# Kernel tuning notes

Measured on AMD Instinct MI355X. Metric: run time of the kernel, lower is better.

## Reference

```python
import jax, jax.numpy as jnp
import numpy as np

K = 7
PAD = (K - 1) // 2  # padding=None branch in __init__
STRIDE = 1
N, C, P, H, W = 32, 256, 256, 7, 7


def setup_inputs() -> dict:
    key = jax.random.key(0)
    k1, k2, k3, k4 = jax.random.split(key, 4)
    x = jax.random.normal(k1, (N, C, H, W), dtype=jnp.float32)
    # conv_k = Conv2d(1, planes, 1): weight (P,1,1,1) -> vector Wk, bias bk
    Wk = jax.random.normal(k2, (P,), dtype=jnp.float32) * 0.1
    bk = jax.random.normal(k3, (P,), dtype=jnp.float32) * 0.1
    # conv_adap_kernel bias (its weight is overwritten every forward)
    b_adap = jax.random.normal(k4, (P,), dtype=jnp.float32) * 0.1
    return {"x": x, "Wk": Wk, "bk": bk, "b_adap": b_adap}


def reference(x, Wk, bk, b_adap):
    # Per-sample generated filter: g_k = conv_k(x[i].view(C,1,H,W)) then permute(1,0,2,3)
    # => w[n, p, c, h, w] = x[n, c, h, w] * Wk[p] + bk[p], shape (N, P, C, H, W)
    w = x[:, None, :, :, :] * Wk[None, :, None, None, None] + bk[None, :, None, None, None]

    def conv_one(xi, wi):
        # xi: (C, H, W); wi: (P, C, H, W) -- kernel spatial size == feature map size
        return jax.lax.conv_general_dilated(
            xi[None], wi,
            window_strides=(STRIDE, STRIDE),
            padding=[(PAD, PAD), (PAD, PAD)],
            dimension_numbers=("NCHW", "OIHW", "NCHW"),
        )[0]

    y = jax.vmap(conv_one)(x, w)  # (N, P, Hout, Wout)
    return y + b_adap[None, :, None, None]
```

## Files before the change

### kernel.cpp

```cpp
#include <hip/hip_runtime.h>


#define HW 49

__global__ __launch_bounds__(1024, 4) void adap_fc_kernel(
    const float* __restrict__ x,
    const float* __restrict__ Wk,
    const float* __restrict__ bk,
    const float* __restrict__ ba,
    float* __restrict__ y)
{
    const int bid  = blockIdx.x;
    const int n    = bid & 31;
    const int pg   = bid >> 5;
    const int t    = threadIdx.x;
    const int lane = t & 63;
    const int wg   = (t >> 6) & 3;
    const int q    = t >> 8;

    __shared__ float lx[256 * HW];
    __shared__ float p1[4][25];
    __shared__ float pz[16][HW];
    __shared__ float zz[HW], s1f[HW], s2[HW];
    __shared__ float lwk[32], lbk[32], lba[32];

    const float4* xn4 = (const float4*)(x + (size_t)n * (256 * HW));
    float4* lx4 = (float4*)lx;
    #pragma unroll
    for (int i = 0; i < 3; ++i) lx4[t + i * 1024] = xn4[t + i * 1024];
    if (t < 64) lx4[t + 3072] = xn4[t + 3072];
    if (t < 32) { const int p = pg * 32 + t; lwk[t] = Wk[p]; lbk[t] = bk[p]; lba[t] = ba[p]; }
    __syncthreads();

    const int c = t & 255;
    float v[HW];
    #pragma unroll
    for (int k = 0; k < HW; ++k) v[k] = lx[c * HW + k];

    #pragma unroll
    for (int l = 0; l < 25; ++l) {
        const int lq = (l < 7) ? 0 : (l < 13) ? 1 : (l < 19) ? 2 : 3;
        if (q == lq) {
            const int dh = (l < 4) ? 0 : (l - 4) / 7 + 1;
            const int dw = (l < 4) ? l : (l - 4) % 7 - 3;
            float a = 0.f;
            #pragma unroll
            for (int i = 0; i < 7; ++i) {
                if (i + dh < 0 || i + dh > 6) continue;
                #pragma unroll
                for (int j = 0; j < 7; ++j) {
                    if (j + dw < 0 || j + dw > 6) continue;
                    a += v[(i + dh) * 7 + (j + dw)] * v[i * 7 + j];
                }
            }
            #pragma unroll
            for (int off = 32; off; off >>= 1) a += __shfl_xor(a, off);
            if (lane == 0) p1[wg][l] = a;
        }
    }

    if (t < 784) {
        const int grp = t / 49, pos = t % 49;
        const float* base = lx + (grp * 16) * HW + pos;
        float a0 = 0.f, a1 = 0.f;
        #pragma unroll
        for (int i = 0; i < 16; i += 2) { a0 += base[i * HW]; a1 += base[(i + 1) * HW]; }
        pz[grp][pos] = a0 + a1;
    }
    __syncthreads();

    if (t < HW) {
        float az = 0.f;
        #pragma unroll
        for (int g = 0; g < 16; ++g) az += pz[g][t];
        zz[t] = az;
        int dh = t / 7 - 3, dw = t % 7 - 3;
        if (dh < 0 || (dh == 0 && dw < 0)) { dh = -dh; dw = -dw; }
        const int l = (dh == 0) ? dw : 4 + (dh - 1) * 7 + (dw + 3);
        s1f[t] = p1[0][l] + p1[1][l] + p1[2][l] + p1[3][l];
    }
    __syncthreads();

    if (t < HW) {
        const int doh = t / 7 - 3, dow = t % 7 - 3;
        const int i0 = max(0, doh), i1 = min(6, 6 + doh);
        const int j0 = max(0, dow), j1 = min(6, 6 + dow);
        float s = 0.f;
        for (int i = i0; i <= i1; ++i)
            for (int j = j0; j <= j1; ++j) s += zz[i * 7 + j];
        s2[t] = s;
    }
    __syncthreads();

    float4* yn4 = (float4*)(y + ((size_t)n * 256 + pg * 32) * HW);
    if (t < 392) {
        float o[4];
        #pragma unroll
        for (int cc = 0; cc < 4; ++cc) {
            const int idx = t * 4 + cc;
            const int p = idx / HW, pos = idx - p * HW;
            o[cc] = lwk[p] * s1f[pos] + lbk[p] * s2[pos] + lba[p];
        }
        yn4[t] = make_float4(o[0], o[1], o[2], o[3]);
    }
}

extern "C" void kernel_launch(void* const* d_in, const int* in_sizes, int n_in,
                              void* d_out, int out_size, void* d_ws, size_t ws_size,
                              hipStream_t stream) {
    const float* x  = (const float*)d_in[0];
    const float* Wk = (const float*)d_in[1];
    const float* bk = (const float*)d_in[2];
    const float* ba = (const float*)d_in[3];
    float* y = (float*)d_out;

    adap_fc_kernel<<<256, 1024, 0, stream>>>(x, Wk, bk, ba, y);
}
```

Baseline: 12.56 us.

## Split per-sample reductions into channel-partitioned partial kernel plus epilogue kernel

The single kernel, which had every block redundantly load and reduce all 256 channels of its sample, is split into two launches. The first kernel gives each block 32 channels of a sample, computes the autocorrelation and channel-sum partials, and writes them to workspace. The second kernel sums the 8 partials per sample and applies the separable box sum and the output affine. This removes the 8x redundant reduction work across p-groups, at the cost of an extra kernel launch and a global workspace round trip.

```diff
diff --git a/kernel.cpp b/kernel.cpp
--- a/kernel.cpp
+++ b/kernel.cpp
@@ -3,44 +3,33 @@
 
 #define HW 49
 
-__global__ __launch_bounds__(1024, 4) void adap_fc_kernel(
+__global__ __launch_bounds__(1024, 4) void k1_partials(
     const float* __restrict__ x,
-    const float* __restrict__ Wk,
-    const float* __restrict__ bk,
-    const float* __restrict__ ba,
-    float* __restrict__ y)
+    float* __restrict__ ws)
 {
-    const int bid  = blockIdx.x;
-    const int n    = bid & 31;
-    const int pg   = bid >> 5;
-    const int t    = threadIdx.x;
+    const int bid = blockIdx.x;
+    const int n = bid & 31, g = bid >> 5;
+    const int t = threadIdx.x;
     const int lane = t & 63;
-    const int wg   = (t >> 6) & 3;
-    const int q    = t >> 8;
+    const int sub = t >> 6;
 
-    __shared__ float lx[256 * HW];
-    __shared__ float p1[4][25];
-    __shared__ float pz[16][HW];
-    __shared__ float zz[HW], s1f[HW], s2[HW];
-    __shared__ float lwk[32], lbk[32], lba[32];
+    __shared__ float lx[32 * HW];
 
-    const float4* xn4 = (const float4*)(x + (size_t)n * (256 * HW));
-    float4* lx4 = (float4*)lx;
-    #pragma unroll
-    for (int i = 0; i < 3; ++i) lx4[t + i * 1024] = xn4[t + i * 1024];
-    if (t < 64) lx4[t + 3072] = xn4[t + 3072];
-    if (t < 32) { const int p = pg * 32 + t; lwk[t] = Wk[p]; lbk[t] = bk[p]; lba[t] = ba[p]; }
+    const float4* xs = (const float4*)(x + ((size_t)n * 256 + g * 32) * HW);
+    if (t < 392) ((float4*)lx)[t] = xs[t];
     __syncthreads();
 
-    const int c = t & 255;
+    const int c = lane & 31;
     float v[HW];
     #pragma unroll
     for (int k = 0; k < HW; ++k) v[k] = lx[c * HW + k];
 
+    float* wbase = ws + (size_t)(n * 8 + g) * 80;
+
     #pragma unroll
     for (int l = 0; l < 25; ++l) {
-        const int lq = (l < 7) ? 0 : (l < 13) ? 1 : (l < 19) ? 2 : 3;
-        if (q == lq) {
+        const int own = (l < 16) ? l : (l - 16);
+        if (sub == own) {
             const int dh = (l < 4) ? 0 : (l - 4) / 7 + 1;
             const int dw = (l < 4) ? l : (l - 4) % 7 - 3;
             float a = 0.f;
@@ -54,40 +43,66 @@
                 }
             }
             #pragma unroll
-            for (int off = 32; off; off >>= 1) a += __shfl_xor(a, off);
-            if (lane == 0) p1[wg][l] = a;
+            for (int off = 1; off <= 16; off <<= 1) a += __shfl_xor(a, off);
+            if (lane == 0) wbase[l] = a;
         }
     }
 
-    if (t < 784) {
-        const int grp = t / 49, pos = t % 49;
-        const float* base = lx + (grp * 16) * HW + pos;
-        float a0 = 0.f, a1 = 0.f;
+    #pragma unroll
+    for (int p = 0; p < 49; ++p) {
+        const int own = (p / 3 > 15) ? 15 : (p / 3);
+        if (sub == own) {
+            float a = v[p];
+            #pragma unroll
+            for (int off = 1; off <= 16; off <<= 1) a += __shfl_xor(a, off);
+            if (lane == 32) wbase[25 + p] = a;
+        }
+    }
+}
+
+__global__ __launch_bounds__(512) void k2_epilogue(
+    const float* __restrict__ ws,
+    const float* __restrict__ Wk,
+    const float* __restrict__ bk,
+    const float* __restrict__ ba,
+    float* __restrict__ y)
+{
+    const int bid = blockIdx.x;
+    const int n = bid & 31, pg = bid >> 5;
+    const int t = threadIdx.x;
+
+    __shared__ float sm[80];
+    __shared__ float rs[HW];
+    __shared__ float s1f[HW], s2[HW];
+    __shared__ float lwk[32], lbk[32], lba[32];
+
+    if (t < 32) { const int p = pg * 32 + t; lwk[t] = Wk[p]; lbk[t] = bk[p]; lba[t] = ba[p]; }
+    if (t < 74) {
+        const float* wb = ws + (size_t)n * 8 * 80 + t;
+        float a = 0.f;
         #pragma unroll
-        for (int i = 0; i < 16; i += 2) { a0 += base[i * HW]; a1 += base[(i + 1) * HW]; }
-        pz[grp][pos] = a0 + a1;
+        for (int g = 0; g < 8; ++g) a += wb[g * 80];
+        sm[t] = a;
     }
     __syncthreads();
 
     if (t < HW) {
-        float az = 0.f;
-        #pragma unroll
-        for (int g = 0; g < 16; ++g) az += pz[g][t];
-        zz[t] = az;
         int dh = t / 7 - 3, dw = t % 7 - 3;
         if (dh < 0 || (dh == 0 && dw < 0)) { dh = -dh; dw = -dw; }
-        const int l = (dh == 0) ? dw : 4 + (dh - 1) * 7 + (dw + 3);
-        s1f[t] = p1[0][l] + p1[1][l] + p1[2][l] + p1[3][l];
+        s1f[t] = sm[(dh == 0) ? dw : 4 + (dh - 1) * 7 + (dw + 3)];
+        const int i = t / 7, ow = t % 7;
+        const int j0 = (ow - 3 < 0) ? 0 : ow - 3, j1 = (ow + 3 > 6) ? 6 : ow + 3;
+        float r = 0.f;
+        for (int j = j0; j <= j1; ++j) r += sm[25 + i * 7 + j];
+        rs[t] = r;
     }
     __syncthreads();
 
     if (t < HW) {
-        const int doh = t / 7 - 3, dow = t % 7 - 3;
-        const int i0 = max(0, doh), i1 = min(6, 6 + doh);
-        const int j0 = max(0, dow), j1 = min(6, 6 + dow);
+        const int oh = t / 7, ow = t % 7;
+        const int i0 = (oh - 3 < 0) ? 0 : oh - 3, i1 = (oh + 3 > 6) ? 6 : oh + 3;
         float s = 0.f;
-        for (int i = i0; i <= i1; ++i)
-            for (int j = j0; j <= j1; ++j) s += zz[i * 7 + j];
+        for (int i = i0; i <= i1; ++i) s += rs[i * 7 + ow];
         s2[t] = s;
     }
     __syncthreads();
@@ -112,7 +127,9 @@
     const float* Wk = (const float*)d_in[1];
     const float* bk = (const float*)d_in[2];
     const float* ba = (const float*)d_in[3];
-    float* y = (float*)d_out;
+    float* y  = (float*)d_out;
+    float* ws = (float*)d_ws;
 
-    adap_fc_kernel<<<256, 1024, 0, stream>>>(x, Wk, bk, ba, y);
+    k1_partials<<<256, 1024, 0, stream>>>(x, ws);
+    k2_epilogue<<<256, 512, 0, stream>>>(ws, Wk, bk, ba, y);
 }
```

Measured after the change: 12.20 us (median of 2 runs). 2.9% less time.
